# Performance work log

Hardware: AMD Instinct MI355X
Metric: run time of the kernel (lower is better)

The kernel has to match this reference:

```python
import jax, jax.numpy as jnp
import numpy as np

B, S, D = 2, 2048, 768
NH, GH = 12, 4
HD = D // NH            # 64
GD = HD * GH            # 256 (grouped KV projection width)
REP = NH // GH          # 3  (repeat factor for KV heads)
SCALE = HD ** -0.5
MASK_FILL = -1e-09      # faithful to the original (NOT -1e9)


def setup_inputs() -> dict:
    key = jax.random.key(0)
    ks = jax.random.split(key, 9)
    init = 0.02
    x = jax.random.normal(ks[0], (B, S, D), dtype=jnp.float32)
    masks = jnp.tril(jnp.ones((S, S), dtype=jnp.float32)) > 0  # bool causal mask
    Wq = jax.random.normal(ks[1], (D, D), dtype=jnp.float32) * init
    bq = jnp.zeros((D,), dtype=jnp.float32)
    Wk = jax.random.normal(ks[2], (D, GD), dtype=jnp.float32) * init
    bk = jnp.zeros((GD,), dtype=jnp.float32)
    Wv = jax.random.normal(ks[3], (D, GD), dtype=jnp.float32) * init
    bv = jnp.zeros((GD,), dtype=jnp.float32)
    Wo = jax.random.normal(ks[4], (D, D), dtype=jnp.float32) * init
    bo = jnp.zeros((D,), dtype=jnp.float32)
    return {"x": x, "masks": masks, "Wq": Wq, "bq": bq, "Wk": Wk, "bk": bk,
            "Wv": Wv, "bv": bv, "Wo": Wo, "bo": bo}


def reference(x, masks, Wq, bq, Wk, bk, Wv, bv, Wo, bo):
    bs, seq, _ = x.shape
    # projections (weights stored [in, out])
    q = (x @ Wq + bq).reshape(bs, seq, NH, HD).transpose(0, 2, 1, 3)   # [b, nh, s, hd]
    k = (x @ Wk + bk).reshape(bs, seq, GH, HD).transpose(0, 2, 1, 3)   # [b, gh, s, hd]
    v = (x @ Wv + bv).reshape(bs, seq, GH, HD).transpose(0, 2, 1, 3)
    # repeat_interleave KV heads to match query heads (faithful to original)
    k = jnp.repeat(k, REP, axis=1)                                     # [b, nh, s, hd]
    v = jnp.repeat(v, REP, axis=1)
    scores = jnp.einsum('bhqd,bhkd->bhqk', q, k) * SCALE               # [b, nh, s, s]
    # original: masked_fill(masks == 0, -1e-09)
    scores = jnp.where(masks, scores, MASK_FILL)
    attn = jax.nn.softmax(scores, axis=-1)
    out = jnp.einsum('bhqk,bhkd->bhqd', attn, v)                       # [b, nh, s, hd]
    # faithful to original buggy merge: transpose(-1,-2).contiguous().view(b, s, dim)
    out = out.transpose(0, 1, 3, 2).reshape(bs, seq, D)
    return out @ Wo + bo
```

## Files before the change

### kernel.cpp

```cpp
#include <hip/hip_runtime.h>
#include <hip/hip_bf16.h>
#include <stdint.h>


typedef unsigned short ushort_t;
typedef short bf16x8 __attribute__((ext_vector_type(8)));
typedef float f32x4 __attribute__((ext_vector_type(4)));

#define MFMA(a, b, c) __builtin_amdgcn_mfma_f32_16x16x32_bf16((a), (b), (c), 0, 0, 0)

__device__ __forceinline__ ushort_t f2bf(float f) {
    union { float f; unsigned u; } v; v.f = f;
    const unsigned r = v.u + 0x7FFFu + ((v.u >> 16) & 1u);
    return (ushort_t)(r >> 16);
}
__device__ __forceinline__ unsigned pk2(float a, float b) {
    __hip_bfloat162 h = __float22bfloat162_rn(make_float2(a, b));
    unsigned u; __builtin_memcpy(&u, &h, 4); return u;
}
__device__ __forceinline__ float bflo(unsigned u) {
    union { unsigned u; float f; } v; v.u = u << 16; return v.f;
}
__device__ __forceinline__ float bfhi(unsigned u) {
    union { unsigned u; float f; } v; v.u = u & 0xFFFF0000u; return v.f;
}

__global__ __launch_bounds__(256) void prep_x(const float* __restrict__ x,
                                              ushort_t* __restrict__ xb) {
    const int i = (blockIdx.x * 256 + threadIdx.x) * 4;
    const float4 v = *(const float4*)(x + i);
    uint2 p;
    p.x = (unsigned)f2bf(v.x) | ((unsigned)f2bf(v.y) << 16);
    p.y = (unsigned)f2bf(v.z) | ((unsigned)f2bf(v.w) << 16);
    *(uint2*)(xb + i) = p;
}

__global__ __launch_bounds__(256) void prep_w(
    const float* __restrict__ Wq, const float* __restrict__ Wk,
    const float* __restrict__ Wv, const float* __restrict__ Wo,
    ushort_t* __restrict__ WqT, ushort_t* __restrict__ WkT,
    ushort_t* __restrict__ WvT, ushort_t* __restrict__ WoT) {
    const int z = blockIdx.z;
    const float* src; ushort_t* dst; int N;
    if (z == 0)      { src = Wq; dst = WqT; N = 768; }
    else if (z == 1) { src = Wk; dst = WkT; N = 256; }
    else if (z == 2) { src = Wv; dst = WvT; N = 256; }
    else             { src = Wo; dst = WoT; N = 768; }
    const int k0 = blockIdx.x * 64, n0 = blockIdx.y * 64;
    if (n0 >= N) return;

    __shared__ float Ts[64][65];
    const int tid = threadIdx.x;
    const int r = tid >> 2, cb = (tid & 3) * 16;
    #pragma unroll
    for (int jj = 0; jj < 4; ++jj) {
        const float4 v = *(const float4*)(src + (k0 + r) * N + n0 + cb + jj * 4);
        Ts[cb + jj * 4 + 0][r] = v.x; Ts[cb + jj * 4 + 1][r] = v.y;
        Ts[cb + jj * 4 + 2][r] = v.z; Ts[cb + jj * 4 + 3][r] = v.w;
    }
    __syncthreads();
    const int n = tid >> 2, kc = (tid & 3) * 16;
    unsigned hbuf[16];
    #pragma unroll
    for (int j = 0; j < 16; ++j) hbuf[j] = f2bf(Ts[n][kc + j]);
    uint4 p0, p1;
    p0.x = hbuf[0] | (hbuf[1] << 16);   p0.y = hbuf[2] | (hbuf[3] << 16);
    p0.z = hbuf[4] | (hbuf[5] << 16);   p0.w = hbuf[6] | (hbuf[7] << 16);
    p1.x = hbuf[8] | (hbuf[9] << 16);   p1.y = hbuf[10] | (hbuf[11] << 16);
    p1.z = hbuf[12] | (hbuf[13] << 16); p1.w = hbuf[14] | (hbuf[15] << 16);
    *(uint4*)(dst + (n0 + n) * 768 + k0 + kc) = p0;
    *(uint4*)(dst + (n0 + n) * 768 + k0 + kc + 8) = p1;
}

__global__ __launch_bounds__(256) void qkv_kernel(
    const ushort_t* __restrict__ xb,
    const ushort_t* __restrict__ WqT, const ushort_t* __restrict__ WkT,
    const ushort_t* __restrict__ WvT,
    const float* __restrict__ bq, const float* __restrict__ bk,
    const float* __restrict__ bv,
    ushort_t* __restrict__ Qb, ushort_t* __restrict__ Kb,
    ushort_t* __restrict__ Vtb) {
    const int ct = blockIdx.x, rt = blockIdx.y;
    const int r0 = rt * 128;
    const ushort_t* WT; const float* bias; int head; int kind;
    if (ct < 12)      { WT = WqT; bias = bq; head = ct;      kind = 0; }
    else if (ct < 16) { WT = WkT; bias = bk; head = ct - 12; kind = 1; }
    else              { WT = WvT; bias = bv; head = ct - 16; kind = 2; }
    const int n0 = head * 64;

    __shared__ uint4 Xs[1024];
    __shared__ uint4 Ws[512];

    const int tid = threadIdx.x;
    const int lane = tid & 63, w = tid >> 6;
    const int quad = lane >> 4, l15 = lane & 15;
    const int srX = tid >> 1, sbX = (tid & 1) * 4;
    const int srW = tid >> 2, sbW = (tid & 3) * 2;

    f32x4 acc[2][4] = {};

    for (int k0 = 0; k0 < 768; k0 += 64) {
        __syncthreads();
        #pragma unroll
        for (int c = 0; c < 4; ++c) {
            const int blk = sbX + c;
            Xs[srX * 8 + (blk ^ (srX & 7))] = *(const uint4*)(xb + (r0 + srX) * 768 + k0 + blk * 8);
        }
        #pragma unroll
        for (int c = 0; c < 2; ++c) {
            const int blk = sbW + c;
            Ws[srW * 8 + (blk ^ (srW & 7))] = *(const uint4*)(WT + (n0 + srW) * 768 + k0 + blk * 8);
        }
        __syncthreads();
        #pragma unroll
        for (int ks = 0; ks < 2; ++ks) {
            const int a0r = 32 * w + l15, a1r = 32 * w + 16 + l15;
            const bf16x8 af0 = *(const bf16x8*)&Xs[a0r * 8 + ((quad + 4 * ks) ^ (a0r & 7))];
            const bf16x8 af1 = *(const bf16x8*)&Xs[a1r * 8 + ((quad + 4 * ks) ^ (a1r & 7))];
            #pragma unroll
            for (int ctt = 0; ctt < 4; ++ctt) {
                const int brow = 16 * ctt + l15;
                const bf16x8 bfr = *(const bf16x8*)&Ws[brow * 8 + ((quad + 4 * ks) ^ (brow & 7))];
                acc[0][ctt] = MFMA(af0, bfr, acc[0][ctt]);
                acc[1][ctt] = MFMA(af1, bfr, acc[1][ctt]);
            }
        }
    }
    #pragma unroll
    for (int half = 0; half < 2; ++half) {
        #pragma unroll
        for (int ctt = 0; ctt < 4; ++ctt) {
            const int cd = ctt * 16 + l15;
            const float bv_ = bias[n0 + cd];
            const int row0 = r0 + 32 * w + 16 * half + quad * 4;
            const int b = row0 >> 11;
            if (kind == 2) {
                const int s0 = row0 & 2047;
                unsigned h[4];
                #pragma unroll
                for (int reg = 0; reg < 4; ++reg) h[reg] = f2bf(acc[half][ctt][reg] + bv_);
                uint2 pkv; pkv.x = h[0] | (h[1] << 16); pkv.y = h[2] | (h[3] << 16);
                *(uint2*)(Vtb + ((b * 4 + head) * 64 + cd) * 2048 + s0) = pkv;
            } else {
                #pragma unroll
                for (int reg = 0; reg < 4; ++reg) {
                    const int row = row0 + reg;
                    const int s = row & 2047;
                    const ushort_t h = f2bf(acc[half][ctt][reg] + bv_);
                    if (kind == 0) Qb[((b * 12 + head) * 2048 + s) * 64 + cd] = h;
                    else           Kb[((b * 4 + head) * 2048 + s) * 64 + cd] = h;
                }
            }
        }
    }
}

__global__ __launch_bounds__(256) void vsuffix_kernel(
    const ushort_t* __restrict__ Vtb, float* __restrict__ Vsuf) {
    const int bg = blockIdx.x;
    const int tid = threadIdx.x;
    const int d = tid & 63, part = tid >> 6;
    __shared__ float ts[32][64];
    const ushort_t* base = Vtb + (bg * 64 + d) * 2048;
    for (int t = part * 8; t < part * 8 + 8; ++t) {
        float sum = 0.f;
        #pragma unroll
        for (int j8 = 0; j8 < 8; ++j8) {
            const uint4 v = *(const uint4*)(base + t * 64 + j8 * 8);
            sum += bflo(v.x) + bfhi(v.x) + bflo(v.y) + bfhi(v.y)
                 + bflo(v.z) + bfhi(v.z) + bflo(v.w) + bfhi(v.w);
        }
        ts[t][d] = sum;
    }
    __syncthreads();
    if (tid < 64) {
        float acc = 0.f;
        Vsuf[(bg * 33 + 32) * 64 + tid] = 0.f;
        for (int t = 31; t >= 0; --t) {
            acc += ts[t][tid];
            Vsuf[(bg * 33 + t) * 64 + tid] = acc;
        }
    }
}

__global__ __launch_bounds__(256) void attn_kernel(
    const ushort_t* __restrict__ Qb, const ushort_t* __restrict__ Kb,
    const ushort_t* __restrict__ Vtb, const float* __restrict__ Vsuf,
    ushort_t* __restrict__ aT_hi, ushort_t* __restrict__ aT_lo) {
    const int qt = 31 - blockIdx.x, h = blockIdx.y, b = blockIdx.z;
    const int g = h / 3;
    const int bg = b * 4 + g;
    const int q0 = qt * 64;
    const int tid = threadIdx.x;
    const int lane = tid & 63, w = tid >> 6;
    const int quad = lane >> 4, l15 = lane & 15;

    __shared__ uint4 K_l[512];
    __shared__ uint4 V_l[512];
    __shared__ __align__(16) ushort_t P_l[64 * 72];

    const ushort_t* Qp = Qb + ((b * 12 + h) * 2048 + q0 + 16 * w + l15) * 64;
    const bf16x8 qf0 = *(const bf16x8*)(Qp + quad * 8);
    const bf16x8 qf1 = *(const bf16x8*)(Qp + 32 + quad * 8);

    const ushort_t* Kp = Kb + bg * 2048 * 64;
    const ushort_t* Vp = Vtb + bg * 64 * 2048;

    f32x4 o[4] = {{0,0,0,0},{0,0,0,0},{0,0,0,0},{0,0,0,0}};
    float lsum = 0.f;

    const int sr = tid >> 2, sb = (tid & 3) * 2;
    const int thr = 16 * w + l15;
    ushort_t* Prow = P_l + (16 * w + l15) * 72;

    for (int k0 = 0; k0 <= q0; k0 += 64) {
        __syncthreads();
        #pragma unroll
        for (int c = 0; c < 2; ++c) {
            const int blk = sb + c;
            K_l[sr * 8 + (blk ^ (sr & 7))] = *(const uint4*)(Kp + (k0 + sr) * 64 + blk * 8);
            V_l[sr * 8 + (blk ^ (sr & 7))] = *(const uint4*)(Vp + sr * 2048 + k0 + blk * 8);
        }
        __syncthreads();
        if (k0 < q0) {
            #pragma unroll
            for (int ctt = 0; ctt < 4; ++ctt) {
                const int key = ctt * 16 + l15;
                f32x4 s = {0, 0, 0, 0};
                s = MFMA(*(const bf16x8*)&K_l[key * 8 + ((quad + 0) ^ (key & 7))], qf0, s);
                s = MFMA(*(const bf16x8*)&K_l[key * 8 + ((quad + 4) ^ (key & 7))], qf1, s);
                const float e0 = __expf(s[0] * 0.125f), e1 = __expf(s[1] * 0.125f);
                const float e2 = __expf(s[2] * 0.125f), e3 = __expf(s[3] * 0.125f);
                lsum += (e0 + e1) + (e2 + e3);
                uint2 pw; pw.x = pk2(e0, e1); pw.y = pk2(e2, e3);
                *(uint2*)(Prow + ctt * 16 + quad * 4) = pw;
            }
        } else {
            #pragma unroll
            for (int ctt = 0; ctt < 4; ++ctt) {
                const int key = ctt * 16 + l15;
                f32x4 s = {0, 0, 0, 0};
                s = MFMA(*(const bf16x8*)&K_l[key * 8 + ((quad + 0) ^ (key & 7))], qf0, s);
                s = MFMA(*(const bf16x8*)&K_l[key * 8 + ((quad + 4) ^ (key & 7))], qf1, s);
                const int base = ctt * 16 + quad * 4;
                float e[4];
                #pragma unroll
                for (int reg = 0; reg < 4; ++reg) {
                    const float sv = (base + reg <= thr) ? s[reg] * 0.125f : -1e-9f;
                    e[reg] = __expf(sv);
                    lsum += e[reg];
                }
                uint2 pw; pw.x = pk2(e[0], e[1]); pw.y = pk2(e[2], e[3]);
                *(uint2*)(Prow + ctt * 16 + quad * 4) = pw;
            }
        }
        const bf16x8 pf0 = *(const bf16x8*)&P_l[(16 * w + l15) * 72 + quad * 8];
        const bf16x8 pf1 = *(const bf16x8*)&P_l[(16 * w + l15) * 72 + 32 + quad * 8];
        #pragma unroll
        for (int ctt = 0; ctt < 4; ++ctt) {
            const int d = ctt * 16 + l15;
            o[ctt] = MFMA(pf0, *(const bf16x8*)&V_l[d * 8 + ((quad + 0) ^ (d & 7))], o[ctt]);
            o[ctt] = MFMA(pf1, *(const bf16x8*)&V_l[d * 8 + ((quad + 4) ^ (d & 7))], o[ctt]);
        }
    }
    float ls = lsum;
    ls += __shfl_xor(ls, 16); ls += __shfl_xor(ls, 32);
    const float invv = 1.f / (ls + (float)(1984 - q0));
    float inv_r[4];
    #pragma unroll
    for (int reg = 0; reg < 4; ++reg) inv_r[reg] = __shfl(invv, quad * 4 + reg);
    const float* vsp = Vsuf + (bg * 33 + qt + 1) * 64;
    const int t0 = q0 + 16 * w + quad * 4;
    #pragma unroll
    for (int ctt = 0; ctt < 4; ++ctt) {
        const int d = ctt * 16 + l15;
        const float vs = vsp[d];
        unsigned hh[4], hl[4];
        #pragma unroll
        for (int reg = 0; reg < 4; ++reg) {
            const float val = (o[ctt][reg] + vs) * inv_r[reg];
            const ushort_t hi = f2bf(val);
            union { unsigned u; float f; } vv; vv.u = (unsigned)hi << 16;
            hh[reg] = hi;
            hl[reg] = f2bf(val - vv.f);
        }
        const int idx = (b * 768 + h * 64 + d) * 2048 + t0;
        uint2 ph, pl;
        ph.x = hh[0] | (hh[1] << 16); ph.y = hh[2] | (hh[3] << 16);
        pl.x = hl[0] | (hl[1] << 16); pl.y = hl[2] | (hl[3] << 16);
        *(uint2*)(aT_hi + idx) = ph;
        *(uint2*)(aT_lo + idx) = pl;
    }
}

__global__ __launch_bounds__(256) void out_proj_kernel(
    const ushort_t* __restrict__ aT_hi, const ushort_t* __restrict__ aT_lo,
    const ushort_t* __restrict__ WoT, const float* __restrict__ bo,
    float* __restrict__ out) {
    const int ct = blockIdx.x, rt = blockIdx.y;
    const int r0 = rt * 128, c0 = ct * 64;
    __shared__ uint4 Ah[1024];
    __shared__ uint4 Al[1024];
    __shared__ uint4 Ws[512];
    const int tid = threadIdx.x;
    const int lane = tid & 63, w = tid >> 6;
    const int quad = lane >> 4, l15 = lane & 15;
    const int srX = tid >> 1, sbX = (tid & 1) * 4;
    const int srW = tid >> 2, sbW = (tid & 3) * 2;

    f32x4 acc[2][4] = {};

    for (int k0 = 0; k0 < 768; k0 += 64) {
        __syncthreads();
        #pragma unroll
        for (int c = 0; c < 4; ++c) {
            const int blk = sbX + c;
            const int slot = srX * 8 + (blk ^ (srX & 7));
            Ah[slot] = *(const uint4*)(aT_hi + (r0 + srX) * 768 + k0 + blk * 8);
            Al[slot] = *(const uint4*)(aT_lo + (r0 + srX) * 768 + k0 + blk * 8);
        }
        #pragma unroll
        for (int c = 0; c < 2; ++c) {
            const int blk = sbW + c;
            Ws[srW * 8 + (blk ^ (srW & 7))] = *(const uint4*)(WoT + (c0 + srW) * 768 + k0 + blk * 8);
        }
        __syncthreads();
        #pragma unroll
        for (int ks = 0; ks < 2; ++ks) {
            const int a0r = 32 * w + l15, a1r = 32 * w + 16 + l15;
            const int s0 = a0r * 8 + ((quad + 4 * ks) ^ (a0r & 7));
            const int s1 = a1r * 8 + ((quad + 4 * ks) ^ (a1r & 7));
            const bf16x8 ah0 = *(const bf16x8*)&Ah[s0];
            const bf16x8 ah1 = *(const bf16x8*)&Ah[s1];
            const bf16x8 al0 = *(const bf16x8*)&Al[s0];
            const bf16x8 al1 = *(const bf16x8*)&Al[s1];
            #pragma unroll
            for (int ctt = 0; ctt < 4; ++ctt) {
                const int brow = 16 * ctt + l15;
                const bf16x8 bfr = *(const bf16x8*)&Ws[brow * 8 + ((quad + 4 * ks) ^ (brow & 7))];
                acc[0][ctt] = MFMA(ah0, bfr, acc[0][ctt]);
                acc[0][ctt] = MFMA(al0, bfr, acc[0][ctt]);
                acc[1][ctt] = MFMA(ah1, bfr, acc[1][ctt]);
                acc[1][ctt] = MFMA(al1, bfr, acc[1][ctt]);
            }
        }
    }
    #pragma unroll
    for (int half = 0; half < 2; ++half) {
        #pragma unroll
        for (int ctt = 0; ctt < 4; ++ctt) {
            const int cd = c0 + ctt * 16 + l15;
            const float bo_v = bo[cd];
            #pragma unroll
            for (int reg = 0; reg < 4; ++reg) {
                const int row = r0 + 32 * w + 16 * half + quad * 4 + reg;
                out[row * 768 + cd] = acc[half][ctt][reg] + bo_v;
            }
        }
    }
}

extern "C" void kernel_launch(void* const* d_in, const int* in_sizes, int n_in,
                              void* d_out, int out_size, void* d_ws, size_t ws_size,
                              hipStream_t stream) {
    const float* x  = (const float*)d_in[0];
    const float* Wq = (const float*)d_in[2];
    const float* bq = (const float*)d_in[3];
    const float* Wk = (const float*)d_in[4];
    const float* bk = (const float*)d_in[5];
    const float* Wv = (const float*)d_in[6];
    const float* bv = (const float*)d_in[7];
    const float* Wo = (const float*)d_in[8];
    const float* bo = (const float*)d_in[9];
    float* out = (float*)d_out;

    uint8_t* wsb = (uint8_t*)d_ws;
    ushort_t* xb    = (ushort_t*)(wsb);
    ushort_t* WqT   = (ushort_t*)(wsb + 6291456);
    ushort_t* WkT   = (ushort_t*)(wsb + 7471104);
    ushort_t* WvT   = (ushort_t*)(wsb + 7864320);
    ushort_t* WoT   = (ushort_t*)(wsb + 8257536);
    ushort_t* Qb    = (ushort_t*)(wsb + 9437184);
    ushort_t* Kb    = (ushort_t*)(wsb + 15728640);
    ushort_t* Vtb   = (ushort_t*)(wsb + 17825792);
    float*    Vsuf  = (float*)   (wsb + 19922944);
    ushort_t* aT_hi = (ushort_t*)(wsb + 19990528);
    ushort_t* aT_lo = (ushort_t*)(wsb + 26281984);

    prep_x<<<3072, 256, 0, stream>>>(x, xb);
    prep_w<<<dim3(12, 12, 4), 256, 0, stream>>>(Wq, Wk, Wv, Wo, WqT, WkT, WvT, WoT);
    qkv_kernel<<<dim3(20, 32), 256, 0, stream>>>(xb, WqT, WkT, WvT, bq, bk, bv, Qb, Kb, Vtb);
    vsuffix_kernel<<<8, 256, 0, stream>>>(Vtb, Vsuf);
    attn_kernel<<<dim3(32, 12, 2), 256, 0, stream>>>(Qb, Kb, Vtb, Vsuf, aT_hi, aT_lo);
    out_proj_kernel<<<dim3(12, 32), 256, 0, stream>>>(aT_hi, aT_lo, WoT, bo, out);
}
```

Baseline: 208.1 us.

## Drop LDS staging; load MFMA operands directly from global memory

The QKV projection, attention and output projection kernels no longer stage tiles through shared memory with barriers. Each wave now loads its MFMA fragments straight from global memory and relies on the L1/L2 caches for reuse. The GEMM kernels also shrink row tiles from 128 to 64 and double the grid. The aim is to remove LDS traffic and __syncthreads stalls and to raise occupancy, at the cost of redundant, less coalesced global loads: each K/V/weight fragment is fetched separately by every wave.

```diff
diff --git a/kernel.cpp b/kernel.cpp
--- a/kernel.cpp
+++ b/kernel.cpp
@@ -81,75 +81,55 @@
     ushort_t* __restrict__ Qb, ushort_t* __restrict__ Kb,
     ushort_t* __restrict__ Vtb) {
     const int ct = blockIdx.x, rt = blockIdx.y;
-    const int r0 = rt * 128;
-    const ushort_t* WT; const float* bias; int head; int kind;
+    const int r0 = rt * 64;
+    const ushort_t* WT; const float* bias; int head, kind;
     if (ct < 12)      { WT = WqT; bias = bq; head = ct;      kind = 0; }
     else if (ct < 16) { WT = WkT; bias = bk; head = ct - 12; kind = 1; }
     else              { WT = WvT; bias = bv; head = ct - 16; kind = 2; }
     const int n0 = head * 64;
 
-    __shared__ uint4 Xs[1024];
-    __shared__ uint4 Ws[512];
-
     const int tid = threadIdx.x;
     const int lane = tid & 63, w = tid >> 6;
     const int quad = lane >> 4, l15 = lane & 15;
-    const int srX = tid >> 1, sbX = (tid & 1) * 4;
-    const int srW = tid >> 2, sbW = (tid & 3) * 2;
-
-    f32x4 acc[2][4] = {};
+
+    const ushort_t* ap  = xb + (r0 + 16 * w + l15) * 768 + quad * 8;
+    const ushort_t* bp0 = WT + (n0 + l15) * 768 + quad * 8;
+
+    f32x4 acc[4] = {{0,0,0,0},{0,0,0,0},{0,0,0,0},{0,0,0,0}};
 
     for (int k0 = 0; k0 < 768; k0 += 64) {
-        __syncthreads();
-        #pragma unroll
-        for (int c = 0; c < 4; ++c) {
-            const int blk = sbX + c;
-            Xs[srX * 8 + (blk ^ (srX & 7))] = *(const uint4*)(xb + (r0 + srX) * 768 + k0 + blk * 8);
-        }
-        #pragma unroll
-        for (int c = 0; c < 2; ++c) {
-            const int blk = sbW + c;
-            Ws[srW * 8 + (blk ^ (srW & 7))] = *(const uint4*)(WT + (n0 + srW) * 768 + k0 + blk * 8);
-        }
-        __syncthreads();
         #pragma unroll
         for (int ks = 0; ks < 2; ++ks) {
-            const int a0r = 32 * w + l15, a1r = 32 * w + 16 + l15;
-            const bf16x8 af0 = *(const bf16x8*)&Xs[a0r * 8 + ((quad + 4 * ks) ^ (a0r & 7))];
-            const bf16x8 af1 = *(const bf16x8*)&Xs[a1r * 8 + ((quad + 4 * ks) ^ (a1r & 7))];
+            const bf16x8 af = *(const bf16x8*)(ap + k0 + 32 * ks);
             #pragma unroll
             for (int ctt = 0; ctt < 4; ++ctt) {
-                const int brow = 16 * ctt + l15;
-                const bf16x8 bfr = *(const bf16x8*)&Ws[brow * 8 + ((quad + 4 * ks) ^ (brow & 7))];
-                acc[0][ctt] = MFMA(af0, bfr, acc[0][ctt]);
-                acc[1][ctt] = MFMA(af1, bfr, acc[1][ctt]);
-            }
-        }
-    }
-    #pragma unroll
-    for (int half = 0; half < 2; ++half) {
-        #pragma unroll
-        for (int ctt = 0; ctt < 4; ++ctt) {
-            const int cd = ctt * 16 + l15;
-            const float bv_ = bias[n0 + cd];
-            const int row0 = r0 + 32 * w + 16 * half + quad * 4;
-            const int b = row0 >> 11;
-            if (kind == 2) {
-                const int s0 = row0 & 2047;
-                unsigned h[4];
-                #pragma unroll
-                for (int reg = 0; reg < 4; ++reg) h[reg] = f2bf(acc[half][ctt][reg] + bv_);
-                uint2 pkv; pkv.x = h[0] | (h[1] << 16); pkv.y = h[2] | (h[3] << 16);
-                *(uint2*)(Vtb + ((b * 4 + head) * 64 + cd) * 2048 + s0) = pkv;
-            } else {
-                #pragma unroll
-                for (int reg = 0; reg < 4; ++reg) {
-                    const int row = row0 + reg;
-                    const int s = row & 2047;
-                    const ushort_t h = f2bf(acc[half][ctt][reg] + bv_);
-                    if (kind == 0) Qb[((b * 12 + head) * 2048 + s) * 64 + cd] = h;
-                    else           Kb[((b * 4 + head) * 2048 + s) * 64 + cd] = h;
-                }
+                const bf16x8 bfr = *(const bf16x8*)(bp0 + ctt * 16 * 768 + k0 + 32 * ks);
+                acc[ctt] = MFMA(af, bfr, acc[ctt]);
+            }
+        }
+    }
+
+    const int row0 = r0 + 16 * w + quad * 4;
+    const int b = row0 >> 11;
+    #pragma unroll
+    for (int ctt = 0; ctt < 4; ++ctt) {
+        const int cd = ctt * 16 + l15;
+        const float bv_ = bias[n0 + cd];
+        if (kind == 2) {
+            const int s0 = row0 & 2047;
+            unsigned hh[4];
+            #pragma unroll
+            for (int reg = 0; reg < 4; ++reg) hh[reg] = f2bf(acc[ctt][reg] + bv_);
+            uint2 pkv; pkv.x = hh[0] | (hh[1] << 16); pkv.y = hh[2] | (hh[3] << 16);
+            *(uint2*)(Vtb + ((b * 4 + head) * 64 + cd) * 2048 + s0) = pkv;
+        } else {
+            #pragma unroll
+            for (int reg = 0; reg < 4; ++reg) {
+                const int row = row0 + reg;
+                const int s = row & 2047;
+                const ushort_t hv = f2bf(acc[ctt][reg] + bv_);
+                if (kind == 0) Qb[((b * 12 + head) * 2048 + s) * 64 + cd] = hv;
+                else           Kb[((b * 4 + head) * 2048 + s) * 64 + cd] = hv;
             }
         }
     }
@@ -195,8 +175,6 @@
     const int lane = tid & 63, w = tid >> 6;
     const int quad = lane >> 4, l15 = lane & 15;
 
-    __shared__ uint4 K_l[512];
-    __shared__ uint4 V_l[512];
     __shared__ __align__(16) ushort_t P_l[64 * 72];
 
     const ushort_t* Qp = Qb + ((b * 12 + h) * 2048 + q0 + 16 * w + l15) * 64;
@@ -208,27 +186,18 @@
 
     f32x4 o[4] = {{0,0,0,0},{0,0,0,0},{0,0,0,0},{0,0,0,0}};
     float lsum = 0.f;
-
-    const int sr = tid >> 2, sb = (tid & 3) * 2;
     const int thr = 16 * w + l15;
     ushort_t* Prow = P_l + (16 * w + l15) * 72;
 
     for (int k0 = 0; k0 <= q0; k0 += 64) {
-        __syncthreads();
-        #pragma unroll
-        for (int c = 0; c < 2; ++c) {
-            const int blk = sb + c;
-            K_l[sr * 8 + (blk ^ (sr & 7))] = *(const uint4*)(Kp + (k0 + sr) * 64 + blk * 8);
-            V_l[sr * 8 + (blk ^ (sr & 7))] = *(const uint4*)(Vp + sr * 2048 + k0 + blk * 8);
-        }
-        __syncthreads();
         if (k0 < q0) {
             #pragma unroll
             for (int ctt = 0; ctt < 4; ++ctt) {
                 const int key = ctt * 16 + l15;
+                const ushort_t* kp = Kp + (k0 + key) * 64 + quad * 8;
                 f32x4 s = {0, 0, 0, 0};
-                s = MFMA(*(const bf16x8*)&K_l[key * 8 + ((quad + 0) ^ (key & 7))], qf0, s);
-                s = MFMA(*(const bf16x8*)&K_l[key * 8 + ((quad + 4) ^ (key & 7))], qf1, s);
+                s = MFMA(*(const bf16x8*)kp, qf0, s);
+                s = MFMA(*(const bf16x8*)(kp + 32), qf1, s);
                 const float e0 = __expf(s[0] * 0.125f), e1 = __expf(s[1] * 0.125f);
                 const float e2 = __expf(s[2] * 0.125f), e3 = __expf(s[3] * 0.125f);
                 lsum += (e0 + e1) + (e2 + e3);
@@ -239,9 +208,10 @@
             #pragma unroll
             for (int ctt = 0; ctt < 4; ++ctt) {
                 const int key = ctt * 16 + l15;
+                const ushort_t* kp = Kp + (k0 + key) * 64 + quad * 8;
                 f32x4 s = {0, 0, 0, 0};
-                s = MFMA(*(const bf16x8*)&K_l[key * 8 + ((quad + 0) ^ (key & 7))], qf0, s);
-                s = MFMA(*(const bf16x8*)&K_l[key * 8 + ((quad + 4) ^ (key & 7))], qf1, s);
+                s = MFMA(*(const bf16x8*)kp, qf0, s);
+                s = MFMA(*(const bf16x8*)(kp + 32), qf1, s);
                 const int base = ctt * 16 + quad * 4;
                 float e[4];
                 #pragma unroll
@@ -254,13 +224,14 @@
                 *(uint2*)(Prow + ctt * 16 + quad * 4) = pw;
             }
         }
-        const bf16x8 pf0 = *(const bf16x8*)&P_l[(16 * w + l15) * 72 + quad * 8];
-        const bf16x8 pf1 = *(const bf16x8*)&P_l[(16 * w + l15) * 72 + 32 + quad * 8];
+        const bf16x8 pf0 = *(const bf16x8*)(Prow + quad * 8);
+        const bf16x8 pf1 = *(const bf16x8*)(Prow + 32 + quad * 8);
         #pragma unroll
         for (int ctt = 0; ctt < 4; ++ctt) {
             const int d = ctt * 16 + l15;
-            o[ctt] = MFMA(pf0, *(const bf16x8*)&V_l[d * 8 + ((quad + 0) ^ (d & 7))], o[ctt]);
-            o[ctt] = MFMA(pf1, *(const bf16x8*)&V_l[d * 8 + ((quad + 4) ^ (d & 7))], o[ctt]);
+            const ushort_t* vp = Vp + d * 2048 + k0 + quad * 8;
+            o[ctt] = MFMA(pf0, *(const bf16x8*)vp, o[ctt]);
+            o[ctt] = MFMA(pf1, *(const bf16x8*)(vp + 32), o[ctt]);
         }
     }
     float ls = lsum;
@@ -298,65 +269,38 @@
     const ushort_t* __restrict__ WoT, const float* __restrict__ bo,
     float* __restrict__ out) {
     const int ct = blockIdx.x, rt = blockIdx.y;
-    const int r0 = rt * 128, c0 = ct * 64;
-    __shared__ uint4 Ah[1024];
-    __shared__ uint4 Al[1024];
-    __shared__ uint4 Ws[512];
+    const int r0 = rt * 64, c0 = ct * 64;
     const int tid = threadIdx.x;
     const int lane = tid & 63, w = tid >> 6;
     const int quad = lane >> 4, l15 = lane & 15;
-    const int srX = tid >> 1, sbX = (tid & 1) * 4;
-    const int srW = tid >> 2, sbW = (tid & 3) * 2;
-
-    f32x4 acc[2][4] = {};
+
+    const ushort_t* ahp = aT_hi + (r0 + 16 * w + l15) * 768 + quad * 8;
+    const ushort_t* alp = aT_lo + (r0 + 16 * w + l15) * 768 + quad * 8;
+    const ushort_t* bp0 = WoT + (c0 + l15) * 768 + quad * 8;
+
+    f32x4 acc[4] = {{0,0,0,0},{0,0,0,0},{0,0,0,0},{0,0,0,0}};
 
     for (int k0 = 0; k0 < 768; k0 += 64) {
-        __syncthreads();
-        #pragma unroll
-        for (int c = 0; c < 4; ++c) {
-            const int blk = sbX + c;
-            const int slot = srX * 8 + (blk ^ (srX & 7));
-            Ah[slot] = *(const uint4*)(aT_hi + (r0 + srX) * 768 + k0 + blk * 8);
-            Al[slot] = *(const uint4*)(aT_lo + (r0 + srX) * 768 + k0 + blk * 8);
-        }
-        #pragma unroll
-        for (int c = 0; c < 2; ++c) {
-            const int blk = sbW + c;
-            Ws[srW * 8 + (blk ^ (srW & 7))] = *(const uint4*)(WoT + (c0 + srW) * 768 + k0 + blk * 8);
-        }
-        __syncthreads();
         #pragma unroll
         for (int ks = 0; ks < 2; ++ks) {
-            const int a0r = 32 * w + l15, a1r = 32 * w + 16 + l15;
-            const int s0 = a0r * 8 + ((quad + 4 * ks) ^ (a0r & 7));
-            const int s1 = a1r * 8 + ((quad + 4 * ks) ^ (a1r & 7));
-            const bf16x8 ah0 = *(const bf16x8*)&Ah[s0];
-            const bf16x8 ah1 = *(const bf16x8*)&Ah[s1];
-            const bf16x8 al0 = *(const bf16x8*)&Al[s0];
-            const bf16x8 al1 = *(const bf16x8*)&Al[s1];
+            const bf16x8 ah = *(const bf16x8*)(ahp + k0 + 32 * ks);
+            const bf16x8 al = *(const bf16x8*)(alp + k0 + 32 * ks);
             #pragma unroll
             for (int ctt = 0; ctt < 4; ++ctt) {
-                const int brow = 16 * ctt + l15;
-                const bf16x8 bfr = *(const bf16x8*)&Ws[brow * 8 + ((quad + 4 * ks) ^ (brow & 7))];
-                acc[0][ctt] = MFMA(ah0, bfr, acc[0][ctt]);
-                acc[0][ctt] = MFMA(al0, bfr, acc[0][ctt]);
-                acc[1][ctt] = MFMA(ah1, bfr, acc[1][ctt]);
-                acc[1][ctt] = MFMA(al1, bfr, acc[1][ctt]);
-            }
-        }
-    }
-    #pragma unroll
-    for (int half = 0; half < 2; ++half) {
-        #pragma unroll
-        for (int ctt = 0; ctt < 4; ++ctt) {
-            const int cd = c0 + ctt * 16 + l15;
-            const float bo_v = bo[cd];
-            #pragma unroll
-            for (int reg = 0; reg < 4; ++reg) {
-                const int row = r0 + 32 * w + 16 * half + quad * 4 + reg;
-                out[row * 768 + cd] = acc[half][ctt][reg] + bo_v;
-            }
-        }
+                const bf16x8 bfr = *(const bf16x8*)(bp0 + ctt * 16 * 768 + k0 + 32 * ks);
+                acc[ctt] = MFMA(ah, bfr, acc[ctt]);
+                acc[ctt] = MFMA(al, bfr, acc[ctt]);
+            }
+        }
+    }
+    const int row0 = r0 + 16 * w + quad * 4;
+    #pragma unroll
+    for (int ctt = 0; ctt < 4; ++ctt) {
+        const int cd = c0 + ctt * 16 + l15;
+        const float bo_v = bo[cd];
+        #pragma unroll
+        for (int reg = 0; reg < 4; ++reg)
+            out[(row0 + reg) * 768 + cd] = acc[ctt][reg] + bo_v;
     }
 }
 
@@ -389,8 +333,8 @@
 
     prep_x<<<3072, 256, 0, stream>>>(x, xb);
     prep_w<<<dim3(12, 12, 4), 256, 0, stream>>>(Wq, Wk, Wv, Wo, WqT, WkT, WvT, WoT);
-    qkv_kernel<<<dim3(20, 32), 256, 0, stream>>>(xb, WqT, WkT, WvT, bq, bk, bv, Qb, Kb, Vtb);
+    qkv_kernel<<<dim3(20, 64), 256, 0, stream>>>(xb, WqT, WkT, WvT, bq, bk, bv, Qb, Kb, Vtb);
     vsuffix_kernel<<<8, 256, 0, stream>>>(Vtb, Vsuf);
     attn_kernel<<<dim3(32, 12, 2), 256, 0, stream>>>(Qb, Kb, Vtb, Vsuf, aT_hi, aT_lo);
-    out_proj_kernel<<<dim3(12, 32), 256, 0, stream>>>(aT_hi, aT_lo, WoT, bo, out);
-}
+    out_proj_kernel<<<dim3(12, 64), 256, 0, stream>>>(aT_hi, aT_lo, WoT, bo, out);
+}
```

New measurement: 392.9 us. 88.8% more time.

## Fuse all stages into one persistent cooperative kernel with grid syncs

Applied to the files above, without the earlier changes.

Replaces six separate kernel launches with one cooperative persistent kernel of 512 blocks that runs prep, QKV projection, V suffix sums, attention and output projection as job loops separated by grid-wide syncs. This removes launch overhead and inter-kernel gaps. Attention work is paired (job bid and 1023-bid) to balance the causal triangle, and the output projection tile shrinks to 64 rows so it yields more jobs. The cost is grid-sync overhead, a fixed grid that needs two resident blocks per CU, and serial stages where few blocks work, such as the 8-block suffix stage.

```diff
diff --git a/kernel.cpp b/kernel.cpp
--- a/kernel.cpp
+++ b/kernel.cpp
@@ -1,6 +1,9 @@
 #include <hip/hip_runtime.h>
 #include <hip/hip_bf16.h>
+#include <hip/hip_cooperative_groups.h>
 #include <stdint.h>
+
+namespace cg = cooperative_groups;
 
 
 typedef unsigned short ushort_t;
@@ -25,31 +28,35 @@
     union { unsigned u; float f; } v; v.u = u & 0xFFFF0000u; return v.f;
 }
 
-__global__ __launch_bounds__(256) void prep_x(const float* __restrict__ x,
-                                              ushort_t* __restrict__ xb) {
-    const int i = (blockIdx.x * 256 + threadIdx.x) * 4;
-    const float4 v = *(const float4*)(x + i);
-    uint2 p;
-    p.x = (unsigned)f2bf(v.x) | ((unsigned)f2bf(v.y) << 16);
-    p.y = (unsigned)f2bf(v.z) | ((unsigned)f2bf(v.w) << 16);
-    *(uint2*)(xb + i) = p;
-}
-
-__global__ __launch_bounds__(256) void prep_w(
-    const float* __restrict__ Wq, const float* __restrict__ Wk,
-    const float* __restrict__ Wv, const float* __restrict__ Wo,
-    ushort_t* __restrict__ WqT, ushort_t* __restrict__ WkT,
-    ushort_t* __restrict__ WvT, ushort_t* __restrict__ WoT) {
-    const int z = blockIdx.z;
-    const float* src; ushort_t* dst; int N;
-    if (z == 0)      { src = Wq; dst = WqT; N = 768; }
-    else if (z == 1) { src = Wk; dst = WkT; N = 256; }
-    else if (z == 2) { src = Wv; dst = WvT; N = 256; }
-    else             { src = Wo; dst = WoT; N = 768; }
-    const int k0 = blockIdx.x * 64, n0 = blockIdx.y * 64;
-    if (n0 >= N) return;
-
-    __shared__ float Ts[64][65];
+struct Params {
+    const float *x, *Wq, *bq, *Wk, *bk, *Wv, *bv, *Wo, *bo;
+    float* out;
+    ushort_t *xb, *WqT, *WkT, *WvT, *WoT, *Qb, *Kb, *Vtb;
+    float* Vsuf;
+    ushort_t *aT_hi, *aT_lo;
+};
+
+__device__ __forceinline__ void prep_x_job(int jx, const Params& p) {
+    const int tid = threadIdx.x;
+    const int base = jx * 49152;
+    #pragma unroll 4
+    for (int it = 0; it < 48; ++it) {
+        const int i = base + it * 1024 + tid * 4;
+        const float4 v = *(const float4*)(p.x + i);
+        uint2 pk; pk.x = pk2(v.x, v.y); pk.y = pk2(v.z, v.w);
+        *(uint2*)(p.xb + i) = pk;
+    }
+}
+
+__device__ __forceinline__ void prep_w_job(int jw, const Params& p, uint8_t* sm) {
+    const float* src; ushort_t* dst; int N, kt, nt;
+    if (jw < 144)      { src = p.Wq; dst = p.WqT; N = 768; kt = jw / 12;        nt = jw % 12; }
+    else if (jw < 192) { src = p.Wk; dst = p.WkT; N = 256; kt = (jw - 144) / 4; nt = (jw - 144) % 4; }
+    else if (jw < 240) { src = p.Wv; dst = p.WvT; N = 256; kt = (jw - 192) / 4; nt = (jw - 192) % 4; }
+    else               { src = p.Wo; dst = p.WoT; N = 768; kt = (jw - 240) / 12; nt = (jw - 240) % 12; }
+    const int k0 = kt * 64, n0 = nt * 64;
+
+    float (*Ts)[65] = (float(*)[65])sm;
     const int tid = threadIdx.x;
     const int r = tid >> 2, cb = (tid & 3) * 16;
     #pragma unroll
@@ -72,24 +79,17 @@
     *(uint4*)(dst + (n0 + n) * 768 + k0 + kc + 8) = p1;
 }
 
-__global__ __launch_bounds__(256) void qkv_kernel(
-    const ushort_t* __restrict__ xb,
-    const ushort_t* __restrict__ WqT, const ushort_t* __restrict__ WkT,
-    const ushort_t* __restrict__ WvT,
-    const float* __restrict__ bq, const float* __restrict__ bk,
-    const float* __restrict__ bv,
-    ushort_t* __restrict__ Qb, ushort_t* __restrict__ Kb,
-    ushort_t* __restrict__ Vtb) {
-    const int ct = blockIdx.x, rt = blockIdx.y;
+__device__ __forceinline__ void qkv_job(int jq, const Params& p, uint8_t* sm) {
+    const int ct = jq / 32, rt = jq % 32;
     const int r0 = rt * 128;
-    const ushort_t* WT; const float* bias; int head; int kind;
-    if (ct < 12)      { WT = WqT; bias = bq; head = ct;      kind = 0; }
-    else if (ct < 16) { WT = WkT; bias = bk; head = ct - 12; kind = 1; }
-    else              { WT = WvT; bias = bv; head = ct - 16; kind = 2; }
+    const ushort_t* WT; const float* bias; int head, kind;
+    if (ct < 12)      { WT = p.WqT; bias = p.bq; head = ct;      kind = 0; }
+    else if (ct < 16) { WT = p.WkT; bias = p.bk; head = ct - 12; kind = 1; }
+    else              { WT = p.WvT; bias = p.bv; head = ct - 16; kind = 2; }
     const int n0 = head * 64;
 
-    __shared__ uint4 Xs[1024];
-    __shared__ uint4 Ws[512];
+    uint4* Xs = (uint4*)sm;
+    uint4* Ws = (uint4*)(sm + 16384);
 
     const int tid = threadIdx.x;
     const int lane = tid & 63, w = tid >> 6;
@@ -104,7 +104,7 @@
         #pragma unroll
         for (int c = 0; c < 4; ++c) {
             const int blk = sbX + c;
-            Xs[srX * 8 + (blk ^ (srX & 7))] = *(const uint4*)(xb + (r0 + srX) * 768 + k0 + blk * 8);
+            Xs[srX * 8 + (blk ^ (srX & 7))] = *(const uint4*)(p.xb + (r0 + srX) * 768 + k0 + blk * 8);
         }
         #pragma unroll
         for (int c = 0; c < 2; ++c) {
@@ -136,32 +136,30 @@
             const int b = row0 >> 11;
             if (kind == 2) {
                 const int s0 = row0 & 2047;
-                unsigned h[4];
+                unsigned hh[4];
                 #pragma unroll
-                for (int reg = 0; reg < 4; ++reg) h[reg] = f2bf(acc[half][ctt][reg] + bv_);
-                uint2 pkv; pkv.x = h[0] | (h[1] << 16); pkv.y = h[2] | (h[3] << 16);
-                *(uint2*)(Vtb + ((b * 4 + head) * 64 + cd) * 2048 + s0) = pkv;
+                for (int reg = 0; reg < 4; ++reg) hh[reg] = f2bf(acc[half][ctt][reg] + bv_);
+                uint2 pkv; pkv.x = hh[0] | (hh[1] << 16); pkv.y = hh[2] | (hh[3] << 16);
+                *(uint2*)(p.Vtb + ((b * 4 + head) * 64 + cd) * 2048 + s0) = pkv;
             } else {
                 #pragma unroll
                 for (int reg = 0; reg < 4; ++reg) {
                     const int row = row0 + reg;
                     const int s = row & 2047;
-                    const ushort_t h = f2bf(acc[half][ctt][reg] + bv_);
-                    if (kind == 0) Qb[((b * 12 + head) * 2048 + s) * 64 + cd] = h;
-                    else           Kb[((b * 4 + head) * 2048 + s) * 64 + cd] = h;
+                    const ushort_t hv = f2bf(acc[half][ctt][reg] + bv_);
+                    if (kind == 0) p.Qb[((b * 12 + head) * 2048 + s) * 64 + cd] = hv;
+                    else           p.Kb[((b * 4 + head) * 2048 + s) * 64 + cd] = hv;
                 }
             }
         }
     }
 }
 
-__global__ __launch_bounds__(256) void vsuffix_kernel(
-    const ushort_t* __restrict__ Vtb, float* __restrict__ Vsuf) {
-    const int bg = blockIdx.x;
+__device__ __forceinline__ void vsuffix_job(int bg, const Params& p, uint8_t* sm) {
+    float (*ts)[64] = (float(*)[64])sm;
     const int tid = threadIdx.x;
     const int d = tid & 63, part = tid >> 6;
-    __shared__ float ts[32][64];
-    const ushort_t* base = Vtb + (bg * 64 + d) * 2048;
+    const ushort_t* base = p.Vtb + (bg * 64 + d) * 2048;
     for (int t = part * 8; t < part * 8 + 8; ++t) {
         float sum = 0.f;
         #pragma unroll
@@ -175,19 +173,17 @@
     __syncthreads();
     if (tid < 64) {
         float acc = 0.f;
-        Vsuf[(bg * 33 + 32) * 64 + tid] = 0.f;
+        p.Vsuf[(bg * 33 + 32) * 64 + tid] = 0.f;
         for (int t = 31; t >= 0; --t) {
             acc += ts[t][tid];
-            Vsuf[(bg * 33 + t) * 64 + tid] = acc;
-        }
-    }
-}
-
-__global__ __launch_bounds__(256) void attn_kernel(
-    const ushort_t* __restrict__ Qb, const ushort_t* __restrict__ Kb,
-    const ushort_t* __restrict__ Vtb, const float* __restrict__ Vsuf,
-    ushort_t* __restrict__ aT_hi, ushort_t* __restrict__ aT_lo) {
-    const int qt = 31 - blockIdx.x, h = blockIdx.y, b = blockIdx.z;
+            p.Vsuf[(bg * 33 + t) * 64 + tid] = acc;
+        }
+    }
+}
+
+__device__ __forceinline__ void attn_job(int ja, const Params& p, uint8_t* sm) {
+    const int qt = 31 - ja / 24;
+    const int hb = ja % 24, h = hb % 12, b = hb / 12;
     const int g = h / 3;
     const int bg = b * 4 + g;
     const int q0 = qt * 64;
@@ -195,16 +191,16 @@
     const int lane = tid & 63, w = tid >> 6;
     const int quad = lane >> 4, l15 = lane & 15;
 
-    __shared__ uint4 K_l[512];
-    __shared__ uint4 V_l[512];
-    __shared__ __align__(16) ushort_t P_l[64 * 72];
-
-    const ushort_t* Qp = Qb + ((b * 12 + h) * 2048 + q0 + 16 * w + l15) * 64;
+    uint4* K_l = (uint4*)sm;
+    uint4* V_l = (uint4*)(sm + 8192);
+    ushort_t* P_l = (ushort_t*)(sm + 16384);
+
+    const ushort_t* Qp = p.Qb + ((b * 12 + h) * 2048 + q0 + 16 * w + l15) * 64;
     const bf16x8 qf0 = *(const bf16x8*)(Qp + quad * 8);
     const bf16x8 qf1 = *(const bf16x8*)(Qp + 32 + quad * 8);
 
-    const ushort_t* Kp = Kb + bg * 2048 * 64;
-    const ushort_t* Vp = Vtb + bg * 64 * 2048;
+    const ushort_t* Kp = p.Kb + bg * 2048 * 64;
+    const ushort_t* Vp = p.Vtb + bg * 64 * 2048;
 
     f32x4 o[4] = {{0,0,0,0},{0,0,0,0},{0,0,0,0},{0,0,0,0}};
     float lsum = 0.f;
@@ -254,8 +250,8 @@
                 *(uint2*)(Prow + ctt * 16 + quad * 4) = pw;
             }
         }
-        const bf16x8 pf0 = *(const bf16x8*)&P_l[(16 * w + l15) * 72 + quad * 8];
-        const bf16x8 pf1 = *(const bf16x8*)&P_l[(16 * w + l15) * 72 + 32 + quad * 8];
+        const bf16x8 pf0 = *(const bf16x8*)(Prow + quad * 8);
+        const bf16x8 pf1 = *(const bf16x8*)(Prow + 32 + quad * 8);
         #pragma unroll
         for (int ctt = 0; ctt < 4; ++ctt) {
             const int d = ctt * 16 + l15;
@@ -269,7 +265,7 @@
     float inv_r[4];
     #pragma unroll
     for (int reg = 0; reg < 4; ++reg) inv_r[reg] = __shfl(invv, quad * 4 + reg);
-    const float* vsp = Vsuf + (bg * 33 + qt + 1) * 64;
+    const float* vsp = p.Vsuf + (bg * 33 + qt + 1) * 64;
     const int t0 = q0 + 16 * w + quad * 4;
     #pragma unroll
     for (int ctt = 0; ctt < 4; ++ctt) {
@@ -288,109 +284,112 @@
         uint2 ph, pl;
         ph.x = hh[0] | (hh[1] << 16); ph.y = hh[2] | (hh[3] << 16);
         pl.x = hl[0] | (hl[1] << 16); pl.y = hl[2] | (hl[3] << 16);
-        *(uint2*)(aT_hi + idx) = ph;
-        *(uint2*)(aT_lo + idx) = pl;
-    }
-}
-
-__global__ __launch_bounds__(256) void out_proj_kernel(
-    const ushort_t* __restrict__ aT_hi, const ushort_t* __restrict__ aT_lo,
-    const ushort_t* __restrict__ WoT, const float* __restrict__ bo,
-    float* __restrict__ out) {
-    const int ct = blockIdx.x, rt = blockIdx.y;
-    const int r0 = rt * 128, c0 = ct * 64;
-    __shared__ uint4 Ah[1024];
-    __shared__ uint4 Al[1024];
-    __shared__ uint4 Ws[512];
+        *(uint2*)(p.aT_hi + idx) = ph;
+        *(uint2*)(p.aT_lo + idx) = pl;
+    }
+}
+
+__device__ __forceinline__ void out_job(int jo, const Params& p, uint8_t* sm) {
+    const int ct = jo / 64, rt = jo % 64;
+    const int r0 = rt * 64, c0 = ct * 64;
+    uint4* Ah = (uint4*)sm;
+    uint4* Al = (uint4*)(sm + 8192);
+    uint4* Ws = (uint4*)(sm + 16384);
     const int tid = threadIdx.x;
     const int lane = tid & 63, w = tid >> 6;
     const int quad = lane >> 4, l15 = lane & 15;
-    const int srX = tid >> 1, sbX = (tid & 1) * 4;
-    const int srW = tid >> 2, sbW = (tid & 3) * 2;
-
-    f32x4 acc[2][4] = {};
+    const int sr = tid >> 2, sb = (tid & 3) * 2;
+
+    f32x4 acc[4] = {{0,0,0,0},{0,0,0,0},{0,0,0,0},{0,0,0,0}};
 
     for (int k0 = 0; k0 < 768; k0 += 64) {
         __syncthreads();
         #pragma unroll
-        for (int c = 0; c < 4; ++c) {
-            const int blk = sbX + c;
-            const int slot = srX * 8 + (blk ^ (srX & 7));
-            Ah[slot] = *(const uint4*)(aT_hi + (r0 + srX) * 768 + k0 + blk * 8);
-            Al[slot] = *(const uint4*)(aT_lo + (r0 + srX) * 768 + k0 + blk * 8);
-        }
-        #pragma unroll
         for (int c = 0; c < 2; ++c) {
-            const int blk = sbW + c;
-            Ws[srW * 8 + (blk ^ (srW & 7))] = *(const uint4*)(WoT + (c0 + srW) * 768 + k0 + blk * 8);
+            const int blk = sb + c;
+            const int slot = sr * 8 + (blk ^ (sr & 7));
+            Ah[slot] = *(const uint4*)(p.aT_hi + (r0 + sr) * 768 + k0 + blk * 8);
+            Al[slot] = *(const uint4*)(p.aT_lo + (r0 + sr) * 768 + k0 + blk * 8);
+            Ws[slot] = *(const uint4*)(p.WoT + (c0 + sr) * 768 + k0 + blk * 8);
         }
         __syncthreads();
         #pragma unroll
         for (int ks = 0; ks < 2; ++ks) {
-            const int a0r = 32 * w + l15, a1r = 32 * w + 16 + l15;
-            const int s0 = a0r * 8 + ((quad + 4 * ks) ^ (a0r & 7));
-            const int s1 = a1r * 8 + ((quad + 4 * ks) ^ (a1r & 7));
-            const bf16x8 ah0 = *(const bf16x8*)&Ah[s0];
-            const bf16x8 ah1 = *(const bf16x8*)&Ah[s1];
-            const bf16x8 al0 = *(const bf16x8*)&Al[s0];
-            const bf16x8 al1 = *(const bf16x8*)&Al[s1];
+            const int arow = 16 * w + l15;
+            const int aslot = arow * 8 + ((quad + 4 * ks) ^ (arow & 7));
+            const bf16x8 ah = *(const bf16x8*)&Ah[aslot];
+            const bf16x8 al = *(const bf16x8*)&Al[aslot];
             #pragma unroll
             for (int ctt = 0; ctt < 4; ++ctt) {
                 const int brow = 16 * ctt + l15;
                 const bf16x8 bfr = *(const bf16x8*)&Ws[brow * 8 + ((quad + 4 * ks) ^ (brow & 7))];
-                acc[0][ctt] = MFMA(ah0, bfr, acc[0][ctt]);
-                acc[0][ctt] = MFMA(al0, bfr, acc[0][ctt]);
-                acc[1][ctt] = MFMA(ah1, bfr, acc[1][ctt]);
-                acc[1][ctt] = MFMA(al1, bfr, acc[1][ctt]);
-            }
-        }
-    }
-    #pragma unroll
-    for (int half = 0; half < 2; ++half) {
-        #pragma unroll
-        for (int ctt = 0; ctt < 4; ++ctt) {
-            const int cd = c0 + ctt * 16 + l15;
-            const float bo_v = bo[cd];
-            #pragma unroll
-            for (int reg = 0; reg < 4; ++reg) {
-                const int row = r0 + 32 * w + 16 * half + quad * 4 + reg;
-                out[row * 768 + cd] = acc[half][ctt][reg] + bo_v;
-            }
-        }
-    }
+                acc[ctt] = MFMA(ah, bfr, acc[ctt]);
+                acc[ctt] = MFMA(al, bfr, acc[ctt]);
+            }
+        }
+    }
+    #pragma unroll
+    for (int ctt = 0; ctt < 4; ++ctt) {
+        const int cd = c0 + ctt * 16 + l15;
+        const float bo_v = p.bo[cd];
+        #pragma unroll
+        for (int reg = 0; reg < 4; ++reg) {
+            const int row = r0 + 16 * w + quad * 4 + reg;
+            p.out[row * 768 + cd] = acc[ctt][reg] + bo_v;
+        }
+    }
+}
+
+__global__ __launch_bounds__(256, 2) void fused_kernel(Params p) {
+    __shared__ __align__(16) uint8_t sm[25600];
+    cg::grid_group grid = cg::this_grid();
+    const int bid = blockIdx.x;
+
+    if (bid < 64)       prep_x_job(bid, p);
+    else if (bid < 448) prep_w_job(bid - 64, p, sm);
+    grid.sync();
+
+    for (int j = bid; j < 640; j += 512) qkv_job(j, p, sm);
+    grid.sync();
+
+    if (bid < 8) vsuffix_job(bid, p, sm);
+    grid.sync();
+
+    attn_job(bid, p, sm);
+    if (bid >= 256) attn_job(1023 - bid, p, sm);
+    grid.sync();
+
+    for (int j = bid; j < 768; j += 512) out_job(j, p, sm);
 }
 
 extern "C" void kernel_launch(void* const* d_in, const int* in_sizes, int n_in,
                               void* d_out, int out_size, void* d_ws, size_t ws_size,
                               hipStream_t stream) {
-    const float* x  = (const float*)d_in[0];
-    const float* Wq = (const float*)d_in[2];
-    const float* bq = (const float*)d_in[3];
-    const float* Wk = (const float*)d_in[4];
-    const float* bk = (const float*)d_in[5];
-    const float* Wv = (const float*)d_in[6];
-    const float* bv = (const float*)d_in[7];
-    const float* Wo = (const float*)d_in[8];
-    const float* bo = (const float*)d_in[9];
-    float* out = (float*)d_out;
-
     uint8_t* wsb = (uint8_t*)d_ws;
-    ushort_t* xb    = (ushort_t*)(wsb);
-    ushort_t* WqT   = (ushort_t*)(wsb + 6291456);
-    ushort_t* WkT   = (ushort_t*)(wsb + 7471104);
-    ushort_t* WvT   = (ushort_t*)(wsb + 7864320);
-    ushort_t* WoT   = (ushort_t*)(wsb + 8257536);
-    ushort_t* Qb    = (ushort_t*)(wsb + 9437184);
-    ushort_t* Kb    = (ushort_t*)(wsb + 15728640);
-    ushort_t* Vtb   = (ushort_t*)(wsb + 17825792);
-    float*    Vsuf  = (float*)   (wsb + 19922944);
-    ushort_t* aT_hi = (ushort_t*)(wsb + 19990528);
-    ushort_t* aT_lo = (ushort_t*)(wsb + 26281984);
-
-    prep_x<<<3072, 256, 0, stream>>>(x, xb);
-    prep_w<<<dim3(12, 12, 4), 256, 0, stream>>>(Wq, Wk, Wv, Wo, WqT, WkT, WvT, WoT);
-    qkv_kernel<<<dim3(20, 32), 256, 0, stream>>>(xb, WqT, WkT, WvT, bq, bk, bv, Qb, Kb, Vtb);
-    vsuffix_kernel<<<8, 256, 0, stream>>>(Vtb, Vsuf);
-    attn_kernel<<<dim3(32, 12, 2), 256, 0, stream>>>(Qb, Kb, Vtb, Vsuf, aT_hi, aT_lo);
-    out_proj_kernel<<<dim3(12, 32), 256, 0, stream>>>(aT_hi, aT_lo, WoT, bo, out);
-}
+    Params prm;
+    prm.x  = (const float*)d_in[0];
+    prm.Wq = (const float*)d_in[2];
+    prm.bq = (const float*)d_in[3];
+    prm.Wk = (const float*)d_in[4];
+    prm.bk = (const float*)d_in[5];
+    prm.Wv = (const float*)d_in[6];
+    prm.bv = (const float*)d_in[7];
+    prm.Wo = (const float*)d_in[8];
+    prm.bo = (const float*)d_in[9];
+    prm.out = (float*)d_out;
+    prm.xb    = (ushort_t*)(wsb);
+    prm.WqT   = (ushort_t*)(wsb + 6291456);
+    prm.WkT   = (ushort_t*)(wsb + 7471104);
+    prm.WvT   = (ushort_t*)(wsb + 7864320);
+    prm.WoT   = (ushort_t*)(wsb + 8257536);
+    prm.Qb    = (ushort_t*)(wsb + 9437184);
+    prm.Kb    = (ushort_t*)(wsb + 15728640);
+    prm.Vtb   = (ushort_t*)(wsb + 17825792);
+    prm.Vsuf  = (float*)   (wsb + 19922944);
+    prm.aT_hi = (ushort_t*)(wsb + 19990528);
+    prm.aT_lo = (ushort_t*)(wsb + 26281984);
+
+    void* kargs[] = { (void*)&prm };
+    hipLaunchCooperativeKernel((const void*)fused_kernel, dim3(512), dim3(256),
+                               kargs, 0, stream);
+}
```

Result: slower. 462.4 us (+122.2%).
